# Kernel tuning notes

Hardware: AMD Instinct MI355X
Metric: run time of the kernel (lower is better)

## Reference

```python
import jax, jax.numpy as jnp
import numpy as np

B, T, d, D = 256, 1024, 4, 32  # batch, seqlen, physical dim, bond dim


def setup_inputs() -> dict:
    key = jax.random.key(0)
    k1, k2, k3, k4 = jax.random.split(key, 4)
    X = jax.random.randint(k1, (B, T), 0, d)  # categorical sequences
    k_core = (d * D * D) ** -0.5
    k_vec = d ** -0.5
    # 'noisy' init: ones + 0.5*gaussian, scaled as in __init__
    core = (k_core * (1.0 + 0.5 * jax.random.normal(k2, (d, D, D)))).astype(jnp.float32)
    left_boundary = (k_vec * (1.0 + 0.5 * jax.random.normal(k3, (D,)))).astype(jnp.float32)
    right_boundary = (k_vec * (1.0 + 0.5 * jax.random.normal(k4, (D,)))).astype(jnp.float32)
    return {"X": X, "core": core, "left_boundary": left_boundary,
            "right_boundary": right_boundary}


def reference(X, core, left_boundary, right_boundary):
    """Batched _log_contract_at: log P(x) per sequence via sequential TT
    contraction with infinity-norm rescaling at every step.
    Returns logprobs of shape [B]."""
    batch = X.shape[0]
    Z0 = jnp.max(jnp.abs(left_boundary))  # vec_norm (inf norm)
    v0 = jnp.broadcast_to(left_boundary / Z0, (batch, D))
    acc0 = jnp.full((batch,), jnp.log(Z0), dtype=left_boundary.dtype)

    def step(carry, x_t):
        v, acc = carry
        M = core[x_t]                              # [B, D, D] gathered cores
        v2 = jnp.einsum('bi,bij->bj', v, M)        # running contraction
        Z = jnp.max(jnp.abs(v2), axis=1)           # per-seq inf norm
        return (v2 / Z[:, None], acc + jnp.log(Z)), None

    (v, acc), _ = jax.lax.scan(step, (v0, acc0), X.T)  # scan over seqlen
    out = jnp.einsum('bi,i->b', v, right_boundary)
    # original: log((exp(acc)*out).abs()**2) == 2*(acc + log|out|)
    logprobs = 2.0 * (acc + jnp.log(jnp.abs(out)))
    return logprobs
```

## Files before the change

kernel.cpp:

```cpp
#include <hip/hip_runtime.h>
#include <math.h>


#define TT_B 256
#define TT_T 1024

typedef __attribute__((ext_vector_type(8))) short bf16x8;
typedef __attribute__((ext_vector_type(4))) float f32x4;

__device__ uint4 g_QT[256 * 2 * 64];
__device__ int   g_kQ[256];

__device__ __forceinline__ unsigned pkbf16(float lo, float hi)
{
    unsigned r;
    asm volatile("v_cvt_pk_bf16_f32 %0, %1, %2" : "=v"(r) : "v"(lo), "v"(hi));
    return r;
}
__device__ __forceinline__ bf16x8 as_bf16x8(int4 v)
{ union { int4 i; bf16x8 h; } u; u.i = v; return u.h; }
__device__ __forceinline__ bf16x8 as_bf16x8u(uint4 v)
{ union { uint4 i; bf16x8 h; } u; u.i = v; return u.h; }

#define MAXD4(D) fmaxf(fmaxf(fabsf(D[0]), fabsf(D[1])), fmaxf(fabsf(D[2]), fabsf(D[3])))

__device__ __forceinline__ int tree_node_lds(const float* __restrict__ Ma,
                                             const float* __restrict__ Mb,
                                             float* __restrict__ Mdst, int lane)
{
    const int p = lane & 15, q = lane >> 4;
    const float4 a00 = *(const float4*)(Mb + p * 36 + 8 * q);
    const float4 a01 = *(const float4*)(Mb + p * 36 + 8 * q + 4);
    const float4 a10 = *(const float4*)(Mb + (16 + p) * 36 + 8 * q);
    const float4 a11 = *(const float4*)(Mb + (16 + p) * 36 + 8 * q + 4);
    int4 aw0, aw1;
    aw0.x = (int)pkbf16(a00.x, a00.y); aw0.y = (int)pkbf16(a00.z, a00.w);
    aw0.z = (int)pkbf16(a01.x, a01.y); aw0.w = (int)pkbf16(a01.z, a01.w);
    aw1.x = (int)pkbf16(a10.x, a10.y); aw1.y = (int)pkbf16(a10.z, a10.w);
    aw1.z = (int)pkbf16(a11.x, a11.y); aw1.w = (int)pkbf16(a11.z, a11.w);
    int4 bw0, bw1;
    bw0.x = (int)pkbf16(Ma[(8*q+0)*36 + p], Ma[(8*q+1)*36 + p]);
    bw0.y = (int)pkbf16(Ma[(8*q+2)*36 + p], Ma[(8*q+3)*36 + p]);
    bw0.z = (int)pkbf16(Ma[(8*q+4)*36 + p], Ma[(8*q+5)*36 + p]);
    bw0.w = (int)pkbf16(Ma[(8*q+6)*36 + p], Ma[(8*q+7)*36 + p]);
    bw1.x = (int)pkbf16(Ma[(8*q+0)*36 + 16 + p], Ma[(8*q+1)*36 + 16 + p]);
    bw1.y = (int)pkbf16(Ma[(8*q+2)*36 + 16 + p], Ma[(8*q+3)*36 + 16 + p]);
    bw1.z = (int)pkbf16(Ma[(8*q+4)*36 + 16 + p], Ma[(8*q+5)*36 + 16 + p]);
    bw1.w = (int)pkbf16(Ma[(8*q+6)*36 + 16 + p], Ma[(8*q+7)*36 + 16 + p]);

    const bf16x8 af0 = as_bf16x8(aw0), af1 = as_bf16x8(aw1);
    const bf16x8 bf0 = as_bf16x8(bw0), bf1 = as_bf16x8(bw1);
    const f32x4 zero = {0.f, 0.f, 0.f, 0.f};
    f32x4 d00 = __builtin_amdgcn_mfma_f32_16x16x32_bf16(af0, bf0, zero, 0, 0, 0);
    f32x4 d01 = __builtin_amdgcn_mfma_f32_16x16x32_bf16(af0, bf1, zero, 0, 0, 0);
    f32x4 d10 = __builtin_amdgcn_mfma_f32_16x16x32_bf16(af1, bf0, zero, 0, 0, 0);
    f32x4 d11 = __builtin_amdgcn_mfma_f32_16x16x32_bf16(af1, bf1, zero, 0, 0, 0);

    float zm = fmaxf(fmaxf(MAXD4(d00), MAXD4(d01)), fmaxf(MAXD4(d10), MAXD4(d11)));
    zm = fmaxf(zm, __shfl_xor(zm,  1));
    zm = fmaxf(zm, __shfl_xor(zm,  2));
    zm = fmaxf(zm, __shfl_xor(zm,  4));
    zm = fmaxf(zm, __shfl_xor(zm,  8));
    zm = fmaxf(zm, __shfl_xor(zm, 16));
    zm = fmaxf(zm, __shfl_xor(zm, 32));
    const int eb = __float_as_int(zm) & 0x7f800000;
    const float s = __int_as_float(0x7F000000 - eb);
#pragma unroll
    for (int t = 0; t < 4; ++t) {
        Mdst[(4*q + t) * 36 + p]           = d00[t] * s;
        Mdst[(4*q + t) * 36 + 16 + p]      = d01[t] * s;
        Mdst[(16 + 4*q + t) * 36 + p]      = d10[t] * s;
        Mdst[(16 + 4*q + t) * 36 + 16 + p] = d11[t] * s;
    }
    return (eb >> 23) - 127;
}


__global__ __launch_bounds__(64) void tt_quad_kernel(const float* __restrict__ core)
{
    __shared__ __align__(16) float Qb[6 * 1152];

    const int m    = blockIdx.x;
    const int lane = threadIdx.x;

    const int ia = (m >> 6) & 3;
    const int ib = (m >> 4) & 3;
    const int ic = (m >> 2) & 3;
    const int id =  m       & 3;

    const int r  = lane >> 1;
    const int hh = (lane & 1) * 16;
#define LOADM(SLOT, IDX) do {                                                 \
        const float4* s4_ = (const float4*)(core + (IDX) * 1024 + r * 32 + hh); \
        float4 v0_ = s4_[0], v1_ = s4_[1], v2_ = s4_[2], v3_ = s4_[3];        \
        float4* d4_ = (float4*)(Qb + (SLOT) * 1152 + r * 36 + hh);            \
        d4_[0] = v0_; d4_[1] = v1_; d4_[2] = v2_; d4_[3] = v3_;               \
    } while (0)
    LOADM(0, ia); LOADM(1, ib); LOADM(2, ic); LOADM(3, id);
#undef LOADM
    __syncthreads();

    const int e1 = tree_node_lds(Qb + 1 * 1152, Qb + 0 * 1152, Qb + 4 * 1152, lane);
    const int e2 = tree_node_lds(Qb + 3 * 1152, Qb + 2 * 1152, Qb + 5 * 1152, lane);
    __syncthreads();
    const int e3 = tree_node_lds(Qb + 5 * 1152, Qb + 4 * 1152, Qb + 0 * 1152, lane);
    __syncthreads();

    const float* Qf = Qb;
    const int h = lane >> 5, j = lane & 31;
    float ssum = 0.f;
#pragma unroll
    for (int rr = 0; rr < 16; ++rr) ssum += fabsf(Qf[(16 * h + rr) * 36 + j]);
    ssum += __shfl_xor(ssum, 32);
    float cm = ssum;
    cm = fmaxf(cm, __shfl_xor(cm,  1));
    cm = fmaxf(cm, __shfl_xor(cm,  2));
    cm = fmaxf(cm, __shfl_xor(cm,  4));
    cm = fmaxf(cm, __shfl_xor(cm,  8));
    cm = fmaxf(cm, __shfl_xor(cm, 16));
    const int eb = __float_as_int(cm) & 0x7f800000;
    const float s = __int_as_float(0x7F000000 - eb);
    if (lane == 0) g_kQ[m] = ((eb >> 23) - 127) + e1 + e2 + e3;

    const int g  = lane >> 4;
    const int jj = lane & 15;
#pragma unroll
    for (int H = 0; H < 2; ++H) {
        const int cb = 16 * H + jj;
        uint4 wf;
        wf.x = pkbf16(s * Qf[(4*g+0)*36 + cb],    s * Qf[(4*g+1)*36 + cb]);
        wf.y = pkbf16(s * Qf[(4*g+2)*36 + cb],    s * Qf[(4*g+3)*36 + cb]);
        wf.z = pkbf16(s * Qf[(16+4*g+0)*36 + cb], s * Qf[(16+4*g+1)*36 + cb]);
        wf.w = pkbf16(s * Qf[(16+4*g+2)*36 + cb], s * Qf[(16+4*g+3)*36 + cb]);
        g_QT[(m * 2 + H) * 64 + lane] = wf;
    }
}


#define LOAD2(UB0, UB1, MIDX) do {                                            \
    const int voff_ = (((MIDX) << 11) | (lane << 4));                         \
    asm volatile("global_load_dwordx4 %0, %1, %2"             : "=v"(UB0) : "v"(voff_), "s"(qtb)); \
    asm volatile("global_load_dwordx4 %0, %1, %2 offset:1024" : "=v"(UB1) : "v"(voff_), "s"(qtb)); \
} while (0)

#define MSTEP(UB0, UB1, MIDX, DO_LAST) do {                                   \
    const bf16x8 sb0 = as_bf16x8u(make_uint4(S0w, S1w, S2w, S3w));            \
    const bf16x8 sb1 = as_bf16x8u(make_uint4(S4w, S5w, S6w, S7w));            \
    asm volatile("s_waitcnt vmcnt(6)" ::: "memory");                          \
    __builtin_amdgcn_sched_barrier(0);                                        \
    const bf16x8 af0 = as_bf16x8(UB0);                                        \
    const bf16x8 af1 = as_bf16x8(UB1);                                        \
    f32x4 d00 = __builtin_amdgcn_mfma_f32_16x16x32_bf16(af0, sb0, zero, 0, 0, 0); \
    f32x4 d01 = __builtin_amdgcn_mfma_f32_16x16x32_bf16(af0, sb1, zero, 0, 0, 0); \
    f32x4 d10 = __builtin_amdgcn_mfma_f32_16x16x32_bf16(af1, sb0, zero, 0, 0, 0); \
    f32x4 d11 = __builtin_amdgcn_mfma_f32_16x16x32_bf16(af1, sb1, zero, 0, 0, 0); \
    LOAD2(UB0, UB1, (MIDX));                                                  \
    if (DO_LAST) {                                                            \
        _Pragma("unroll") for (int u_ = 0; u_ < 4; ++u_) {                    \
            Mseg[(4*g + u_) * 36 + jj]           = d00[u_];                   \
            Mseg[(4*g + u_) * 36 + 16 + jj]      = d01[u_];                   \
            Mseg[(16 + 4*g + u_) * 36 + jj]      = d10[u_];                   \
            Mseg[(16 + 4*g + u_) * 36 + 16 + jj] = d11[u_];                   \
        }                                                                     \
    } else {                                                                  \
        S0w = pkbf16(d00[0], d00[1]);  S1w = pkbf16(d00[2], d00[3]);          \
        S2w = pkbf16(d10[0], d10[1]);  S3w = pkbf16(d10[2], d10[3]);          \
        S4w = pkbf16(d01[0], d01[1]);  S5w = pkbf16(d01[2], d01[3]);          \
        S6w = pkbf16(d11[0], d11[1]);  S7w = pkbf16(d11[2], d11[3]);          \
    }                                                                         \
} while (0)

__global__ __launch_bounds__(1024, 1) void tt_main_kernel(const int* __restrict__ X,
                                                          const float* __restrict__ Lb,
                                                          const float* __restrict__ Rb,
                                                          float* __restrict__ out)
{
    __shared__ __align__(16) int   idxs[272];
    __shared__ __align__(16) float Ms[24 * 1152];
    __shared__ int   EcA[16];
    __shared__ int   kpart[16];

    const int b    = blockIdx.x;
    const int tid  = threadIdx.x;
    const int wid  = tid >> 6;
    const int lane = tid & 63;

    int ksum = 0;
    if (tid < 256) {
        const int4 xv = ((const int4*)(X + (size_t)b * TT_T))[tid];
        const int m = ((xv.x * 4 + xv.y) * 4 + xv.z) * 4 + xv.w;
        idxs[tid] = m;
        ksum = g_kQ[m];
    }
    if (tid >= 256 && tid < 272) idxs[tid] = 0;
    if (tid < 16) EcA[tid] = 0;
    ksum += __shfl_xor(ksum,  1);
    ksum += __shfl_xor(ksum,  2);
    ksum += __shfl_xor(ksum,  4);
    ksum += __shfl_xor(ksum,  8);
    ksum += __shfl_xor(ksum, 16);
    ksum += __shfl_xor(ksum, 32);
    if (lane == 0) kpart[wid] = ksum;
    __syncthreads();

    const uint4* qtb = g_QT;
    const f32x4 zero = {0.f, 0.f, 0.f, 0.f};

    const int base4 = 4 * wid;
    const int4* idxs4 = (const int4*)idxs;
    const int g = lane >> 4, jj = lane & 15;
    float* Mseg = Ms + wid * 1152;

    unsigned S0w, S1w, S2w, S3w, S4w, S5w, S6w, S7w;
    {
        const unsigned e0 = ((4*g+0 == jj) ? 0x3F80u : 0u) | ((4*g+1 == jj) ? 0x3F800000u : 0u);
        const unsigned e1 = ((4*g+2 == jj) ? 0x3F80u : 0u) | ((4*g+3 == jj) ? 0x3F800000u : 0u);
        S0w = e0; S1w = e1; S2w = 0u; S3w = 0u;
        S4w = 0u; S5w = 0u; S6w = e0; S7w = e1;
    }

    int4 Ba0, Ba1, Bb0, Bb1, Bc0, Bc1, Bd0, Bd1;
    {
        const int4 m0 = idxs4[base4];
        LOAD2(Ba0, Ba1, m0.x);
        LOAD2(Bb0, Bb1, m0.y);
        LOAD2(Bc0, Bc1, m0.z);
        LOAD2(Bd0, Bd1, m0.w);
    }
    int4 mqc = idxs4[base4 + 1];

#pragma unroll 1
    for (int J = 0; J < 4; ++J) {
        const int4 mq_nx = idxs4[base4 + J + 2];

        const bool lt = (J == 3);
        MSTEP(Ba0, Ba1, mqc.x, 0);
        MSTEP(Bb0, Bb1, mqc.y, 0);
        MSTEP(Bc0, Bc1, mqc.z, 0);
        MSTEP(Bd0, Bd1, mqc.w, lt);
        mqc = mq_nx;
    }

    asm volatile("s_waitcnt vmcnt(0)" ::: "memory");
    __syncthreads();

    if (wid < 8) {
        const int ec = tree_node_lds(Ms + (2*wid) * 1152, Ms + (2*wid + 1) * 1152,
                                     Ms + (16 + wid) * 1152, lane);
        if (lane == 0) EcA[wid] = ec;
    }
    __syncthreads();
    if (wid < 4) {
        const int ec = tree_node_lds(Ms + (16 + 2*wid) * 1152, Ms + (16 + 2*wid + 1) * 1152,
                                     Ms + wid * 1152, lane);
        if (lane == 0) EcA[8 + wid] = ec;
    }
    __syncthreads();
    if (wid < 2) {
        const int ec = tree_node_lds(Ms + (2*wid) * 1152, Ms + (2*wid + 1) * 1152,
                                     Ms + (16 + wid) * 1152, lane);
        if (lane == 0) EcA[12 + wid] = ec;
    }
    __syncthreads();
    int ecL4 = 0;
    if (wid == 0) {
        ecL4 = tree_node_lds(Ms + 16 * 1152, Ms + 17 * 1152, Ms, lane);
    }

    if (wid == 0 && lane < 32) {
        const float* Mt = Ms;
        float v = 0.f;
#pragma unroll 8
        for (int c2 = 0; c2 < 32; ++c2) v = fmaf(Rb[c2], Mt[c2 * 36 + lane], v);
        float p = v * Lb[lane];
        p += __shfl_xor(p,  1);
        p += __shfl_xor(p,  2);
        p += __shfl_xor(p,  4);
        p += __shfl_xor(p,  8);
        p += __shfl_xor(p, 16);
        if (lane == 0) {
            int S = ecL4;
#pragma unroll
            for (int w = 0; w < 16; ++w) S += EcA[w] + kpart[w];
            out[b] = 2.0f * ((float)S * 0.6931471805599453f + logf(fabsf(p)));
        }
    }
}

extern "C" void kernel_launch(void* const* d_in, const int* in_sizes, int n_in,
                              void* d_out, int out_size, void* d_ws, size_t ws_size,
                              hipStream_t stream)
{
    const int*   X    = (const int*)d_in[0];
    const float* core = (const float*)d_in[1];
    const float* Lb   = (const float*)d_in[2];
    const float* Rb   = (const float*)d_in[3];
    float* out = (float*)d_out;

    tt_quad_kernel<<<dim3(256), dim3(64), 0, stream>>>(core);
    tt_main_kernel<<<dim3(256), dim3(1024), 0, stream>>>(X, Lb, Rb, out);
}
```

Before: 21.45 us.

## Fuse quad precompute into main kernel using per-block pair-product table in LDS

Drops the separate kernel that precomputed 256 four-symbol core products into global memory. Each block now builds the 16 two-symbol products with MFMA into an LDS table and walks 32 pair steps per wave, reading operands from LDS instead of global. This removes one kernel launch and the global round trip, but each wave now does twice as many sequential MFMA steps, and every block recomputes the table.

```diff
diff --git a/kernel.cpp b/kernel.cpp
--- a/kernel.cpp
+++ b/kernel.cpp
@@ -7,9 +7,6 @@
 
 typedef __attribute__((ext_vector_type(8))) short bf16x8;
 typedef __attribute__((ext_vector_type(4))) float f32x4;
-
-__device__ uint4 g_QT[256 * 2 * 64];
-__device__ int   g_kQ[256];
 
 __device__ __forceinline__ unsigned pkbf16(float lo, float hi)
 {
@@ -75,125 +72,107 @@
     return (eb >> 23) - 127;
 }
 
-
-__global__ __launch_bounds__(64) void tt_quad_kernel(const float* __restrict__ core)
-{
-    __shared__ __align__(16) float Qb[6 * 1152];
-
-    const int m    = blockIdx.x;
-    const int lane = threadIdx.x;
-
-    const int ia = (m >> 6) & 3;
-    const int ib = (m >> 4) & 3;
-    const int ic = (m >> 2) & 3;
-    const int id =  m       & 3;
-
-    const int r  = lane >> 1;
-    const int hh = (lane & 1) * 16;
-#define LOADM(SLOT, IDX) do {                                                 \
-        const float4* s4_ = (const float4*)(core + (IDX) * 1024 + r * 32 + hh); \
-        float4 v0_ = s4_[0], v1_ = s4_[1], v2_ = s4_[2], v3_ = s4_[3];        \
-        float4* d4_ = (float4*)(Qb + (SLOT) * 1152 + r * 36 + hh);            \
-        d4_[0] = v0_; d4_[1] = v1_; d4_[2] = v2_; d4_[3] = v3_;               \
-    } while (0)
-    LOADM(0, ia); LOADM(1, ib); LOADM(2, ic); LOADM(3, id);
-#undef LOADM
-    __syncthreads();
-
-    const int e1 = tree_node_lds(Qb + 1 * 1152, Qb + 0 * 1152, Qb + 4 * 1152, lane);
-    const int e2 = tree_node_lds(Qb + 3 * 1152, Qb + 2 * 1152, Qb + 5 * 1152, lane);
-    __syncthreads();
-    const int e3 = tree_node_lds(Qb + 5 * 1152, Qb + 4 * 1152, Qb + 0 * 1152, lane);
-    __syncthreads();
-
-    const float* Qf = Qb;
-    const int h = lane >> 5, j = lane & 31;
-    float ssum = 0.f;
-#pragma unroll
-    for (int rr = 0; rr < 16; ++rr) ssum += fabsf(Qf[(16 * h + rr) * 36 + j]);
-    ssum += __shfl_xor(ssum, 32);
-    float cm = ssum;
-    cm = fmaxf(cm, __shfl_xor(cm,  1));
-    cm = fmaxf(cm, __shfl_xor(cm,  2));
-    cm = fmaxf(cm, __shfl_xor(cm,  4));
-    cm = fmaxf(cm, __shfl_xor(cm,  8));
-    cm = fmaxf(cm, __shfl_xor(cm, 16));
-    const int eb = __float_as_int(cm) & 0x7f800000;
-    const float s = __int_as_float(0x7F000000 - eb);
-    if (lane == 0) g_kQ[m] = ((eb >> 23) - 127) + e1 + e2 + e3;
-
-    const int g  = lane >> 4;
-    const int jj = lane & 15;
-#pragma unroll
-    for (int H = 0; H < 2; ++H) {
-        const int cb = 16 * H + jj;
-        uint4 wf;
-        wf.x = pkbf16(s * Qf[(4*g+0)*36 + cb],    s * Qf[(4*g+1)*36 + cb]);
-        wf.y = pkbf16(s * Qf[(4*g+2)*36 + cb],    s * Qf[(4*g+3)*36 + cb]);
-        wf.z = pkbf16(s * Qf[(16+4*g+0)*36 + cb], s * Qf[(16+4*g+1)*36 + cb]);
-        wf.w = pkbf16(s * Qf[(16+4*g+2)*36 + cb], s * Qf[(16+4*g+3)*36 + cb]);
-        g_QT[(m * 2 + H) * 64 + lane] = wf;
-    }
-}
-
-
-#define LOAD2(UB0, UB1, MIDX) do {                                            \
-    const int voff_ = (((MIDX) << 11) | (lane << 4));                         \
-    asm volatile("global_load_dwordx4 %0, %1, %2"             : "=v"(UB0) : "v"(voff_), "s"(qtb)); \
-    asm volatile("global_load_dwordx4 %0, %1, %2 offset:1024" : "=v"(UB1) : "v"(voff_), "s"(qtb)); \
-} while (0)
-
-#define MSTEP(UB0, UB1, MIDX, DO_LAST) do {                                   \
-    const bf16x8 sb0 = as_bf16x8u(make_uint4(S0w, S1w, S2w, S3w));            \
-    const bf16x8 sb1 = as_bf16x8u(make_uint4(S4w, S5w, S6w, S7w));            \
-    asm volatile("s_waitcnt vmcnt(6)" ::: "memory");                          \
-    __builtin_amdgcn_sched_barrier(0);                                        \
-    const bf16x8 af0 = as_bf16x8(UB0);                                        \
-    const bf16x8 af1 = as_bf16x8(UB1);                                        \
-    f32x4 d00 = __builtin_amdgcn_mfma_f32_16x16x32_bf16(af0, sb0, zero, 0, 0, 0); \
-    f32x4 d01 = __builtin_amdgcn_mfma_f32_16x16x32_bf16(af0, sb1, zero, 0, 0, 0); \
-    f32x4 d10 = __builtin_amdgcn_mfma_f32_16x16x32_bf16(af1, sb0, zero, 0, 0, 0); \
-    f32x4 d11 = __builtin_amdgcn_mfma_f32_16x16x32_bf16(af1, sb1, zero, 0, 0, 0); \
-    LOAD2(UB0, UB1, (MIDX));                                                  \
-    if (DO_LAST) {                                                            \
-        _Pragma("unroll") for (int u_ = 0; u_ < 4; ++u_) {                    \
-            Mseg[(4*g + u_) * 36 + jj]           = d00[u_];                   \
-            Mseg[(4*g + u_) * 36 + 16 + jj]      = d01[u_];                   \
-            Mseg[(16 + 4*g + u_) * 36 + jj]      = d10[u_];                   \
-            Mseg[(16 + 4*g + u_) * 36 + 16 + jj] = d11[u_];                   \
-        }                                                                     \
-    } else {                                                                  \
-        S0w = pkbf16(d00[0], d00[1]);  S1w = pkbf16(d00[2], d00[3]);          \
-        S2w = pkbf16(d10[0], d10[1]);  S3w = pkbf16(d10[2], d10[3]);          \
-        S4w = pkbf16(d01[0], d01[1]);  S5w = pkbf16(d01[2], d01[3]);          \
-        S6w = pkbf16(d11[0], d11[1]);  S7w = pkbf16(d11[2], d11[3]);          \
-    }                                                                         \
-} while (0)
-
-__global__ __launch_bounds__(1024, 1) void tt_main_kernel(const int* __restrict__ X,
-                                                          const float* __restrict__ Lb,
-                                                          const float* __restrict__ Rb,
-                                                          float* __restrict__ out)
-{
-    __shared__ __align__(16) int   idxs[272];
+__global__ __launch_bounds__(1024, 1) void tt_fused_kernel(const int* __restrict__ X,
+                                                           const float* __restrict__ core,
+                                                           const float* __restrict__ Lb,
+                                                           const float* __restrict__ Rb,
+                                                           float* __restrict__ out)
+{
     __shared__ __align__(16) float Ms[24 * 1152];
-    __shared__ int   EcA[16];
-    __shared__ int   kpart[16];
+    __shared__ __align__(16) uint4 Ptab[2048];
+    __shared__ int pidx[544];
+    __shared__ int kP[16];
+    __shared__ int EcA[16];
+    __shared__ int kpart[16];
 
     const int b    = blockIdx.x;
     const int tid  = threadIdx.x;
     const int wid  = tid >> 6;
     const int lane = tid & 63;
+    const int p = lane & 15, q = lane >> 4;
+    const int g = q, jj = p;
+
+    if (tid < 512) {
+        const int2 xv = ((const int2*)(X + (size_t)b * TT_T))[tid];
+        pidx[tid] = xv.x * 4 + xv.y;
+    } else if (tid < 544) {
+        pidx[tid] = 0;
+    }
+    if (tid < 16) EcA[tid] = 0;
+    if (wid >= 8 && wid < 12) {
+        const int mi = wid - 8;
+        const int r = lane >> 1, hh = (lane & 1) * 16;
+        const float4* s4 = (const float4*)(core + mi * 1024 + r * 32 + hh);
+        float4 v0 = s4[0], v1 = s4[1], v2 = s4[2], v3 = s4[3];
+        float4* d4 = (float4*)(Ms + (16 + mi) * 1152 + r * 36 + hh);
+        d4[0] = v0; d4[1] = v1; d4[2] = v2; d4[3] = v3;
+    }
+    __syncthreads();
+
+    const f32x4 zero = {0.f, 0.f, 0.f, 0.f};
+
+    {
+        const float* Pa = Ms + (16 + (wid & 3)) * 1152;
+        const float* Pb = Ms + (16 + (wid >> 2)) * 1152;
+        const float4 a00 = *(const float4*)(Pb + p * 36 + 8 * q);
+        const float4 a01 = *(const float4*)(Pb + p * 36 + 8 * q + 4);
+        const float4 a10 = *(const float4*)(Pb + (16 + p) * 36 + 8 * q);
+        const float4 a11 = *(const float4*)(Pb + (16 + p) * 36 + 8 * q + 4);
+        int4 aw0, aw1;
+        aw0.x = (int)pkbf16(a00.x, a00.y); aw0.y = (int)pkbf16(a00.z, a00.w);
+        aw0.z = (int)pkbf16(a01.x, a01.y); aw0.w = (int)pkbf16(a01.z, a01.w);
+        aw1.x = (int)pkbf16(a10.x, a10.y); aw1.y = (int)pkbf16(a10.z, a10.w);
+        aw1.z = (int)pkbf16(a11.x, a11.y); aw1.w = (int)pkbf16(a11.z, a11.w);
+        int4 bw0, bw1;
+        bw0.x = (int)pkbf16(Pa[(8*q+0)*36 + p], Pa[(8*q+1)*36 + p]);
+        bw0.y = (int)pkbf16(Pa[(8*q+2)*36 + p], Pa[(8*q+3)*36 + p]);
+        bw0.z = (int)pkbf16(Pa[(8*q+4)*36 + p], Pa[(8*q+5)*36 + p]);
+        bw0.w = (int)pkbf16(Pa[(8*q+6)*36 + p], Pa[(8*q+7)*36 + p]);
+        bw1.x = (int)pkbf16(Pa[(8*q+0)*36 + 16 + p], Pa[(8*q+1)*36 + 16 + p]);
+        bw1.y = (int)pkbf16(Pa[(8*q+2)*36 + 16 + p], Pa[(8*q+3)*36 + 16 + p]);
+        bw1.z = (int)pkbf16(Pa[(8*q+4)*36 + 16 + p], Pa[(8*q+5)*36 + 16 + p]);
+        bw1.w = (int)pkbf16(Pa[(8*q+6)*36 + 16 + p], Pa[(8*q+7)*36 + 16 + p]);
+        const bf16x8 af0 = as_bf16x8(aw0), af1 = as_bf16x8(aw1);
+        const bf16x8 bf0 = as_bf16x8(bw0), bf1 = as_bf16x8(bw1);
+        f32x4 d00 = __builtin_amdgcn_mfma_f32_16x16x32_bf16(af0, bf0, zero, 0, 0, 0);
+        f32x4 d01 = __builtin_amdgcn_mfma_f32_16x16x32_bf16(af0, bf1, zero, 0, 0, 0);
+        f32x4 d10 = __builtin_amdgcn_mfma_f32_16x16x32_bf16(af1, bf0, zero, 0, 0, 0);
+        f32x4 d11 = __builtin_amdgcn_mfma_f32_16x16x32_bf16(af1, bf1, zero, 0, 0, 0);
+
+        float rs[4], ru[4];
+#pragma unroll
+        for (int t = 0; t < 4; ++t) {
+            rs[t] = fabsf(d00[t]) + fabsf(d01[t]);
+            ru[t] = fabsf(d10[t]) + fabsf(d11[t]);
+        }
+#pragma unroll
+        for (int sh = 1; sh <= 8; sh <<= 1) {
+#pragma unroll
+            for (int t = 0; t < 4; ++t) {
+                rs[t] += __shfl_xor(rs[t], sh);
+                ru[t] += __shfl_xor(ru[t], sh);
+            }
+        }
+        float mx = fmaxf(fmaxf(fmaxf(rs[0], rs[1]), fmaxf(rs[2], rs[3])),
+                         fmaxf(fmaxf(ru[0], ru[1]), fmaxf(ru[2], ru[3])));
+        mx = fmaxf(mx, __shfl_xor(mx, 16));
+        mx = fmaxf(mx, __shfl_xor(mx, 32));
+        const int eb = __float_as_int(mx) & 0x7f800000;
+        const float s = __int_as_float(0x7F000000 - eb);
+        if (lane == 0) kP[wid] = (eb >> 23) - 127;
+
+        uint4 H0, H1;
+        H0.x = pkbf16(d00[0]*s, d00[1]*s);  H0.y = pkbf16(d00[2]*s, d00[3]*s);
+        H0.z = pkbf16(d10[0]*s, d10[1]*s);  H0.w = pkbf16(d10[2]*s, d10[3]*s);
+        H1.x = pkbf16(d01[0]*s, d01[1]*s);  H1.y = pkbf16(d01[2]*s, d01[3]*s);
+        H1.z = pkbf16(d11[0]*s, d11[1]*s);  H1.w = pkbf16(d11[2]*s, d11[3]*s);
+        Ptab[wid * 128 + lane]      = H0;
+        Ptab[wid * 128 + 64 + lane] = H1;
+    }
+    __syncthreads();
 
     int ksum = 0;
-    if (tid < 256) {
-        const int4 xv = ((const int4*)(X + (size_t)b * TT_T))[tid];
-        const int m = ((xv.x * 4 + xv.y) * 4 + xv.z) * 4 + xv.w;
-        idxs[tid] = m;
-        ksum = g_kQ[m];
-    }
-    if (tid >= 256 && tid < 272) idxs[tid] = 0;
-    if (tid < 16) EcA[tid] = 0;
+    if (tid < 512) ksum = kP[pidx[tid]];
     ksum += __shfl_xor(ksum,  1);
     ksum += __shfl_xor(ksum,  2);
     ksum += __shfl_xor(ksum,  4);
@@ -201,14 +180,8 @@
     ksum += __shfl_xor(ksum, 16);
     ksum += __shfl_xor(ksum, 32);
     if (lane == 0) kpart[wid] = ksum;
-    __syncthreads();
-
-    const uint4* qtb = g_QT;
-    const f32x4 zero = {0.f, 0.f, 0.f, 0.f};
-
-    const int base4 = 4 * wid;
-    const int4* idxs4 = (const int4*)idxs;
-    const int g = lane >> 4, jj = lane & 15;
+
+    const int base = 32 * wid;
     float* Mseg = Ms + wid * 1152;
 
     unsigned S0w, S1w, S2w, S3w, S4w, S5w, S6w, S7w;
@@ -219,29 +192,41 @@
         S4w = 0u; S5w = 0u; S6w = e0; S7w = e1;
     }
 
-    int4 Ba0, Ba1, Bb0, Bb1, Bc0, Bc1, Bd0, Bd1;
-    {
-        const int4 m0 = idxs4[base4];
-        LOAD2(Ba0, Ba1, m0.x);
-        LOAD2(Bb0, Bb1, m0.y);
-        LOAD2(Bc0, Bc1, m0.z);
-        LOAD2(Bd0, Bd1, m0.w);
-    }
-    int4 mqc = idxs4[base4 + 1];
+    const int m0 = pidx[base];
+    uint4 F0c = Ptab[m0 * 128 + lane];
+    uint4 F1c = Ptab[m0 * 128 + 64 + lane];
 
 #pragma unroll 1
-    for (int J = 0; J < 4; ++J) {
-        const int4 mq_nx = idxs4[base4 + J + 2];
-
-        const bool lt = (J == 3);
-        MSTEP(Ba0, Ba1, mqc.x, 0);
-        MSTEP(Bb0, Bb1, mqc.y, 0);
-        MSTEP(Bc0, Bc1, mqc.z, 0);
-        MSTEP(Bd0, Bd1, mqc.w, lt);
-        mqc = mq_nx;
-    }
-
-    asm volatile("s_waitcnt vmcnt(0)" ::: "memory");
+    for (int t = 0; t < 32; ++t) {
+        const int mn = pidx[base + t + 1];
+        const uint4 F0n = Ptab[mn * 128 + lane];
+        const uint4 F1n = Ptab[mn * 128 + 64 + lane];
+
+        const bf16x8 af0 = as_bf16x8u(F0c);
+        const bf16x8 af1 = as_bf16x8u(F1c);
+        const bf16x8 sb0 = as_bf16x8u(make_uint4(S0w, S1w, S2w, S3w));
+        const bf16x8 sb1 = as_bf16x8u(make_uint4(S4w, S5w, S6w, S7w));
+        f32x4 d00 = __builtin_amdgcn_mfma_f32_16x16x32_bf16(af0, sb0, zero, 0, 0, 0);
+        f32x4 d01 = __builtin_amdgcn_mfma_f32_16x16x32_bf16(af0, sb1, zero, 0, 0, 0);
+        f32x4 d10 = __builtin_amdgcn_mfma_f32_16x16x32_bf16(af1, sb0, zero, 0, 0, 0);
+        f32x4 d11 = __builtin_amdgcn_mfma_f32_16x16x32_bf16(af1, sb1, zero, 0, 0, 0);
+
+        if (t == 31) {
+#pragma unroll
+            for (int u = 0; u < 4; ++u) {
+                Mseg[(4*g + u) * 36 + jj]           = d00[u];
+                Mseg[(4*g + u) * 36 + 16 + jj]      = d01[u];
+                Mseg[(16 + 4*g + u) * 36 + jj]      = d10[u];
+                Mseg[(16 + 4*g + u) * 36 + 16 + jj] = d11[u];
+            }
+        } else {
+            S0w = pkbf16(d00[0], d00[1]);  S1w = pkbf16(d00[2], d00[3]);
+            S2w = pkbf16(d10[0], d10[1]);  S3w = pkbf16(d10[2], d10[3]);
+            S4w = pkbf16(d01[0], d01[1]);  S5w = pkbf16(d01[2], d01[3]);
+            S6w = pkbf16(d11[0], d11[1]);  S7w = pkbf16(d11[2], d11[3]);
+        }
+        F0c = F0n; F1c = F1n;
+    }
     __syncthreads();
 
     if (wid < 8) {
@@ -272,17 +257,17 @@
         float v = 0.f;
 #pragma unroll 8
         for (int c2 = 0; c2 < 32; ++c2) v = fmaf(Rb[c2], Mt[c2 * 36 + lane], v);
-        float p = v * Lb[lane];
-        p += __shfl_xor(p,  1);
-        p += __shfl_xor(p,  2);
-        p += __shfl_xor(p,  4);
-        p += __shfl_xor(p,  8);
-        p += __shfl_xor(p, 16);
+        float pp = v * Lb[lane];
+        pp += __shfl_xor(pp,  1);
+        pp += __shfl_xor(pp,  2);
+        pp += __shfl_xor(pp,  4);
+        pp += __shfl_xor(pp,  8);
+        pp += __shfl_xor(pp, 16);
         if (lane == 0) {
             int S = ecL4;
 #pragma unroll
             for (int w = 0; w < 16; ++w) S += EcA[w] + kpart[w];
-            out[b] = 2.0f * ((float)S * 0.6931471805599453f + logf(fabsf(p)));
+            out[b] = 2.0f * ((float)S * 0.6931471805599453f + logf(fabsf(pp)));
         }
     }
 }
@@ -297,6 +282,5 @@
     const float* Rb   = (const float*)d_in[3];
     float* out = (float*)d_out;
 
-    tt_quad_kernel<<<dim3(256), dim3(64), 0, stream>>>(core);
-    tt_main_kernel<<<dim3(256), dim3(1024), 0, stream>>>(X, Lb, Rb, out);
-}
+    tt_fused_kernel<<<dim3(256), dim3(1024), 0, stream>>>(X, core, Lb, Rb, out);
+}
```

Result: faster. 20.97 us (median of 2 runs) (-2.2%).
